# Optimization experiments

Hardware: AMD Instinct MI355X
Metric: run time of the kernel (lower is better)

The kernel has to match this reference:

```python
import jax, jax.numpy as jnp
import numpy as np

B, N, P, E = 64, 512, 256, 4096          # batch, nodes (stations), partition nodes, edges
NUM_NWP, LP, F = 8, 16, 32               # num_nwp, local_points, local_cnn_dims
NT, ED, H, W = 8, 8, 64, 8               # num_temp, edge_feature_dims, decf_mlp_hidden, weight_function_dim
G, RH = 64, 256                          # gnn_dim, readout_hid_dim
H1, Q = 128, 9                           # mlp_hid_dim1, num quantiles


def setup_inputs() -> dict:
    key = jax.random.key(0)
    ks = iter(jax.random.split(key, 40))
    def rn(shape, s=0.05):
        return jax.random.normal(next(ks), shape, dtype=jnp.float32) * s
    # one-hot incidence matrices: each edge has one left (partition) node and one right node
    lidx = jax.random.randint(next(ks), (E,), 0, P)
    ridx = jax.random.randint(next(ks), (E,), 0, N)
    linc = jnp.zeros((P, E), jnp.float32).at[lidx, jnp.arange(E)].set(1.0)
    rinc = jnp.zeros((E, N), jnp.float32).at[jnp.arange(E), ridx].set(1.0)
    inp = {
        "x1": jax.random.normal(next(ks), (B, NUM_NWP * N, LP), dtype=jnp.float32),
        "x2": jax.random.normal(next(ks), (B, NT), dtype=jnp.float32),
        # LocalConv1D grouped conv (torch OIW layout: [Cout, Cin/groups, K])
        "conv_w": rn((F * N, NUM_NWP, LP)), "conv_b": rn((F * N,)),
        # WDSGCN2 edge-weight MLP
        "k1_w": rn((H, ED)), "k1_b": rn((H,)),
        "k2_w": rn((H, NT)),
        "k3_w": rn((H, F)),
        "k4_w": rn((H, F)),
        "k5_w": rn((W, H)), "k5_b": rn((W,)),
        "gc_w": rn((G, F * W)), "gc_b": rn((G,)),
        # readout
        "r0_w": rn((RH, G * P)),
        "r1_w": rn((RH, NT)), "r1_b": rn((RH,)),
        "r2_w": rn((RH, P)),
        "r3_w": rn((P, RH)), "r3_b": rn((P,)),
        # SMlp (forward uses l1 -> ELU -> l3 only)
        "l1_w": rn((H1, NT + G)), "l1_b": rn((H1,)),
        "l3_w": rn((Q, H1)), "l3_b": rn((Q,)),
        # buffers
        "ef": jax.random.normal(next(ks), (E, ED + 1), dtype=jnp.float32),
        "linc": linc,
        "rinc": rinc,
        "cap_feature": jax.random.normal(next(ks), (P,), dtype=jnp.float32),
        "partition_idx": jnp.arange(P, dtype=jnp.int32) * (N // P),
    }
    return inp


def reference(x1, x2, conv_w, conv_b, k1_w, k1_b, k2_w, k3_w, k4_w, k5_w, k5_b,
              gc_w, gc_b, r0_w, r1_w, r1_b, r2_w, r3_w, r3_b,
              l1_w, l1_b, l3_w, l3_b, ef, linc, rinc, cap_feature, partition_idx):
    b = x1.shape[0]
    # --- LocalConv1D: grouped conv1d (valid padding, output length 1) + ReLU ---
    y = jax.lax.conv_general_dilated(x1, conv_w, (1,), 'VALID',
                                     dimension_numbers=('NCH', 'OIH', 'NCH'),
                                     feature_group_count=N)
    x = jax.nn.relu(y + conv_b[None, :, None]).reshape(b, N, F)      # [B,N,F]
    # --- WDSGCN2: per-edge weight kernel ---
    kern = ef[:, :-1] @ k1_w.T + k1_b                                # [E,H]
    kern = kern[None] + (x2 @ k2_w.T)[:, None, :]                    # [B,E,H]
    xp = x[:, partition_idx, :]                                      # [B,P,F]
    kern = kern + jnp.einsum('pe,bpf->bef', linc, xp) @ k3_w.T       # left-node feats
    rx = jnp.einsum('en,bnf->bef', rinc, x)                          # right-node feats [B,E,F]
    kern = kern + rx @ k4_w.T
    kern = jax.nn.relu(jax.nn.leaky_relu(kern, 0.02) @ k5_w.T + k5_b)  # [B,E,W]
    # --- message = kernel (outer) right-node features, aggregated by left incidence ---
    msg = kern[:, :, :, None] * rx[:, :, None, :]                    # [B,E,W,F]
    agg = jnp.einsum('pe,bewf->bpwf', linc, msg).reshape(b, P, W * F)
    yg = jax.nn.relu(agg @ gc_w.T + gc_b)                            # [B,P,G]
    # --- readout attention over partition nodes ---
    h = yg.reshape(b, -1) @ r0_w.T + (x2 @ r1_w.T + r1_b) + cap_feature @ r2_w.T
    wt = jax.nn.relu(jax.nn.leaky_relu(h, 0.01) @ r3_w.T + r3_b)     # [B,P]
    res = jnp.einsum('bp,bpg->bg', wt, yg)                           # [B,G]
    # --- SMlp head ---
    z = jnp.concatenate([res, x2], axis=1)
    z = jax.nn.elu(z @ l1_w.T + l1_b)
    return z @ l3_w.T + l3_b                                         # [B,Q]
```

## Files before the change

kernel.cpp:

```cpp
#include <hip/hip_runtime.h>
#include <math.h>

#define B_ 64
#define N_ 512
#define P_ 256
#define E_ 4096
#define F_ 32
#define H_ 64
#define W_ 8
#define G_ 64
#define RH_ 256

#define X_OFF   0
#define T4_OFF  (X_OFF + N_*B_*F_)
#define T3_OFF  (T4_OFF + N_*B_*H_)
#define KB_OFF  (T3_OFF + P_*B_*H_)
#define KW_OFF  (KB_OFF + E_*H_)
#define YG_OFF  (KW_OFF + E_*B_*W_)
#define HB_OFF  (YG_OFF + B_*P_*G_)
#define RES_OFF (HB_OFF + B_*RH_)
#define INT_OFF (RES_OFF + 4*B_*G_)

__global__ __launch_bounds__(256) void k_decode(const float* __restrict__ linc,
    const float* __restrict__ rinc, int* __restrict__ lidx, int* __restrict__ ridx) {
  int i4 = blockIdx.x * 256 + threadIdx.x;
  const int L4 = (P_ * E_) / 4;
  if (i4 < L4) {
    float4 v = ((const float4*)linc)[i4];
    int i = i4 * 4;
    int p = i >> 12, e = i & 4095;
    if (v.x != 0.0f) lidx[e]     = p;
    if (v.y != 0.0f) lidx[e + 1] = p;
    if (v.z != 0.0f) lidx[e + 2] = p;
    if (v.w != 0.0f) lidx[e + 3] = p;
  } else {
    int j4 = i4 - L4;
    float4 v = ((const float4*)rinc)[j4];
    int j = j4 * 4;
    int e = j >> 9, n = j & 511;
    if (v.x != 0.0f) ridx[e] = n;
    if (v.y != 0.0f) ridx[e] = n + 1;
    if (v.z != 0.0f) ridx[e] = n + 2;
    if (v.w != 0.0f) ridx[e] = n + 3;
  }
}

__global__ __launch_bounds__(1024) void k_lists(const int* __restrict__ lidx,
    int* __restrict__ part_start, int* __restrict__ part_edges) {
  __shared__ int cnt[256];
  __shared__ int buf[256];
  __shared__ int cur[256];
  int t = threadIdx.x;
  if (t < 256) cnt[t] = 0;
  __syncthreads();
  for (int e = t; e < E_; e += 1024) atomicAdd(&cnt[lidx[e]], 1);
  __syncthreads();
  if (t < 256) buf[t] = cnt[t];
  __syncthreads();
  for (int off = 1; off < 256; off <<= 1) {
    int add = 0;
    if (t < 256 && t >= off) add = buf[t - off];
    __syncthreads();
    if (t < 256) buf[t] += add;
    __syncthreads();
  }
  if (t < 256) {
    part_start[t + 1] = buf[t];
    if (t == 0) part_start[0] = 0;
    cur[t] = buf[t] - cnt[t];
  }
  __syncthreads();
  for (int e = t; e < E_; e += 1024) {
    int p = lidx[e];
    int pos = atomicAdd(&cur[p], 1);
    part_edges[pos] = e;
  }
}

__global__ __launch_bounds__(256) void k_conv(const float* __restrict__ x1,
    const float* __restrict__ conv_w, const float* __restrict__ conv_b,
    float* __restrict__ x) {
  __shared__ float wsm[32 * 132];
  __shared__ float xsm[8192];
  int n = blockIdx.x, t = threadIdx.x;
  for (int i = t; i < 1024; i += 256) {
    int f = i >> 5, j = i & 31;
    ((float4*)wsm)[f * 33 + j] = ((const float4*)(conv_w + n * 4096))[i];
  }
  for (int i = t; i < 2048; i += 256) {
    int b = i >> 5, j = i & 31;
    ((float4*)xsm)[i] = ((const float4*)(x1 + b * 65536 + n * 128))[j];
  }
  __syncthreads();
  int f = t & 31, bq = t >> 5;
  float cb = conv_b[n * 32 + f];
  float acc[8];
#pragma unroll
  for (int bi = 0; bi < 8; bi++) acc[bi] = cb;
  const float4* wf4 = (const float4*)wsm + f * 33;
  const float4* xb4 = (const float4*)xsm + bq * 256;
#pragma unroll 4
  for (int k4 = 0; k4 < 32; k4++) {
    float4 wv = wf4[k4];
#pragma unroll
    for (int bi = 0; bi < 8; bi++) {
      float4 xv = xb4[bi * 32 + k4];
      acc[bi] += wv.x * xv.x + wv.y * xv.y + wv.z * xv.z + wv.w * xv.w;
    }
  }
#pragma unroll
  for (int bi = 0; bi < 8; bi++) {
    int b = bq * 8 + bi;
    x[n * 2048 + b * 32 + f] = fmaxf(acc[bi], 0.0f);
  }
}

__global__ __launch_bounds__(256) void k_prep(
    const float* __restrict__ x, const int* __restrict__ pidx,
    const float* __restrict__ k3_w, const float* __restrict__ k4_w,
    const float* __restrict__ x2, const float* __restrict__ k2_w,
    const float* __restrict__ ef, const float* __restrict__ k1_w,
    const float* __restrict__ k1_b,
    const float* __restrict__ r1_w, const float* __restrict__ r1_b,
    const float* __restrict__ r2_w, const float* __restrict__ cap,
    float* __restrict__ t4, float* __restrict__ t3, float* __restrict__ kb,
    float* __restrict__ hbuf) {
  __shared__ float xsh[2048];
  __shared__ float wsh[64 * 36];
  __shared__ float x2s[512];
  __shared__ float k2s[512];
  int blk = blockIdx.x, t = threadIdx.x;
  if (blk < 768) {
    bool isT4 = blk < 512;
    int n = isT4 ? blk : pidx[blk - 512];
    const float* wmat = isT4 ? k4_w : k3_w;
    float* outp = isT4 ? (t4 + blk * 4096) : (t3 + (blk - 512) * 4096);
    for (int i = t; i < 512; i += 256) {
      ((float4*)xsh)[i] = ((const float4*)(x + n * 2048))[i];
      int h = i >> 3, j = i & 7;
      ((float4*)wsh)[h * 9 + j] = ((const float4*)wmat)[i];
    }
    if (isT4) {
      for (int i = t; i < 128; i += 256) {
        ((float4*)x2s)[i] = ((const float4*)x2)[i];
        ((float4*)k2s)[i] = ((const float4*)k2_w)[i];
      }
    }
    __syncthreads();
    int h = t & 63, bq = t >> 6;
    float wreg[32];
#pragma unroll
    for (int j = 0; j < 8; j++) {
      float4 v = ((float4*)wsh)[h * 9 + j];
      wreg[4 * j] = v.x; wreg[4 * j + 1] = v.y; wreg[4 * j + 2] = v.z; wreg[4 * j + 3] = v.w;
    }
    float w2[8];
    if (isT4) {
      float4 u = ((float4*)k2s)[h * 2], v = ((float4*)k2s)[h * 2 + 1];
      w2[0] = u.x; w2[1] = u.y; w2[2] = u.z; w2[3] = u.w;
      w2[4] = v.x; w2[5] = v.y; w2[6] = v.z; w2[7] = v.w;
    }
    for (int bi = 0; bi < 16; bi++) {
      int b = bq * 16 + bi;
      float acc = 0.0f;
#pragma unroll
      for (int j = 0; j < 8; j++) {
        float4 xv = ((float4*)xsh)[b * 8 + j];
        acc += xv.x * wreg[4 * j] + xv.y * wreg[4 * j + 1] +
               xv.z * wreg[4 * j + 2] + xv.w * wreg[4 * j + 3];
      }
      if (isT4) {
        float4 u = ((float4*)x2s)[b * 2], v = ((float4*)x2s)[b * 2 + 1];
        acc += u.x * w2[0] + u.y * w2[1] + u.z * w2[2] + u.w * w2[3] +
               v.x * w2[4] + v.y * w2[5] + v.z * w2[6] + v.w * w2[7];
      }
      outp[b * 64 + h] = acc;
    }
  } else if (blk < 1792) {
    int o = (blk - 768) * 256 + t;
    int e = o >> 6, h = o & 63;
    float acc = k1_b[h];
    const float* er = ef + e * 9;
    const float* kr = k1_w + h * 8;
#pragma unroll
    for (int d = 0; d < 8; d++) acc += er[d] * kr[d];
    kb[o] = acc;
  } else {
    int o = (blk - 1792) * 256 + t;
    int rh = o & 255;
    float acc = r1_b[rh];
    const float* xr = x2 + (o >> 8) * 8;
    const float* rr = r1_w + rh * 8;
#pragma unroll
    for (int d = 0; d < 8; d++) acc += xr[d] * rr[d];
    const float* r2r = r2_w + rh * 256;
    for (int p4 = 0; p4 < 64; p4++) {
      float4 cv = ((const float4*)cap)[p4];
      float4 rv = ((const float4*)r2r)[p4];
      acc += cv.x * rv.x + cv.y * rv.y + cv.z * rv.z + cv.w * rv.w;
    }
    hbuf[o] = acc;
  }
}

__global__ __launch_bounds__(256) void k_eagg(
    const float* __restrict__ x, const float* __restrict__ kb,
    const float* __restrict__ t3, const float* __restrict__ t4,
    const float* __restrict__ k5_w, const float* __restrict__ k5_b,
    const int* __restrict__ ridx, const int* __restrict__ part_start,
    const int* __restrict__ part_edges,
    const float* __restrict__ gc_w, const float* __restrict__ gc_b,
    float* __restrict__ yg) {
  __shared__ float t3s[64 * 68];
  __shared__ float k5t[4 * 520];
  __shared__ unsigned short accS[64 * 256];
  int p = blockIdx.x, t = threadIdx.x;
  for (int i = t; i < 512; i += 256) {
    int h = i >> 3, w = i & 7;
    float v = k5_w[w * 64 + h];
#pragma unroll
    for (int qq = 0; qq < 4; qq++) k5t[qq * 520 + i] = v;
  }
  for (int i4 = t; i4 < 1024; i4 += 256) {
    float4 v = ((const float4*)(t3 + p * 4096))[i4];
    *(float4*)(t3s + (i4 >> 4) * 68 + (i4 & 15) * 4) = v;
  }
  __syncthreads();
  int s = t & 3, b = t >> 2;
  const float* kq = k5t + s * 520 + s * 128;
  float kb5_0 = k5_b[2 * s], kb5_1 = k5_b[2 * s + 1];
  const float4* t3p = (const float4*)(t3s + b * 68 + s * 16);
  float acc[64];
#pragma unroll
  for (int j = 0; j < 64; j++) acc[j] = 0.0f;
  int s0 = part_start[p], s1 = part_start[p + 1];
  int e = 0, r = 0;
  if (s0 < s1) { e = part_edges[s0]; r = ridx[e]; }
  for (int idx = s0; idx < s1; idx++) {
    int e_n = 0, r_n = 0;
    if (idx + 1 < s1) { e_n = part_edges[idx + 1]; r_n = ridx[e_n]; }
    const float4* xp = (const float4*)(x + r * 2048 + b * 32);
    float4 xv0 = xp[0], xv1 = xp[1], xv2 = xp[2], xv3 = xp[3];
    float4 xv4 = xp[4], xv5 = xp[5], xv6 = xp[6], xv7 = xp[7];
    const float4* kb4 = (const float4*)(kb + e * 64 + s * 16);
    const float4* t44 = (const float4*)(t4 + r * 4096 + b * 64 + s * 16);
    float lk[16];
#pragma unroll
    for (int j4 = 0; j4 < 4; j4++) {
      float4 a = kb4[j4], c = t3p[j4], d = t44[j4];
      float v;
      v = a.x + c.x + d.x; lk[j4 * 4 + 0] = v > 0.0f ? v : 0.02f * v;
      v = a.y + c.y + d.y; lk[j4 * 4 + 1] = v > 0.0f ? v : 0.02f * v;
      v = a.z + c.z + d.z; lk[j4 * 4 + 2] = v > 0.0f ? v : 0.02f * v;
      v = a.w + c.w + d.w; lk[j4 * 4 + 3] = v > 0.0f ? v : 0.02f * v;
    }
    float pw[8] = {0, 0, 0, 0, 0, 0, 0, 0};
#pragma unroll
    for (int j = 0; j < 16; j++) {
      float4 u = *(const float4*)(kq + j * 8);
      float4 v = *(const float4*)(kq + j * 8 + 4);
      float l = lk[j];
      pw[0] += l * u.x; pw[1] += l * u.y; pw[2] += l * u.z; pw[3] += l * u.w;
      pw[4] += l * v.x; pw[5] += l * v.y; pw[6] += l * v.z; pw[7] += l * v.w;
    }
#pragma unroll
    for (int w = 0; w < 8; w++) {
      pw[w] += __shfl_xor(pw[w], 1);
      pw[w] += __shfl_xor(pw[w], 2);
    }
    float kv0 = fmaxf(pw[2 * s] + kb5_0, 0.0f);
    float kv1 = fmaxf(pw[2 * s + 1] + kb5_1, 0.0f);
    float xa[32];
    xa[0] = xv0.x; xa[1] = xv0.y; xa[2] = xv0.z; xa[3] = xv0.w;
    xa[4] = xv1.x; xa[5] = xv1.y; xa[6] = xv1.z; xa[7] = xv1.w;
    xa[8] = xv2.x; xa[9] = xv2.y; xa[10] = xv2.z; xa[11] = xv2.w;
    xa[12] = xv3.x; xa[13] = xv3.y; xa[14] = xv3.z; xa[15] = xv3.w;
    xa[16] = xv4.x; xa[17] = xv4.y; xa[18] = xv4.z; xa[19] = xv4.w;
    xa[20] = xv5.x; xa[21] = xv5.y; xa[22] = xv5.z; xa[23] = xv5.w;
    xa[24] = xv6.x; xa[25] = xv6.y; xa[26] = xv6.z; xa[27] = xv6.w;
    xa[28] = xv7.x; xa[29] = xv7.y; xa[30] = xv7.z; xa[31] = xv7.w;
#pragma unroll
    for (int j = 0; j < 32; j++) acc[j] += kv0 * xa[j];
#pragma unroll
    for (int j = 0; j < 32; j++) acc[32 + j] += kv1 * xa[j];
    e = e_n; r = r_n;
  }
#pragma unroll
  for (int o = 0; o < 8; o++) {
    int koct = s * 8 + o;
    int os = koct ^ (b >> 3);
    unsigned int wds[4];
#pragma unroll
    for (int h = 0; h < 4; h++) {
      unsigned int u0 = __float_as_uint(acc[o * 8 + 2 * h]);
      u0 = u0 + 0x7fffu + ((u0 >> 16) & 1u);
      unsigned int u1 = __float_as_uint(acc[o * 8 + 2 * h + 1]);
      u1 = u1 + 0x7fffu + ((u1 >> 16) & 1u);
      wds[h] = (u0 >> 16) | (u1 & 0xffff0000u);
    }
    int4 pk = make_int4((int)wds[0], (int)wds[1], (int)wds[2], (int)wds[3]);
    *(int4*)(accS + b * 256 + os * 8) = pk;
  }
  __syncthreads();
  int lane = t & 63, wv = t >> 6;
  int bg = lane >> 3, gg = lane & 7;
  int g0 = wv * 16 + gg * 2;
  const float* gw0 = gc_w + g0 * 256;
  const float* gw1 = gc_w + (g0 + 1) * 256;
  float ac[8][2];
#pragma unroll
  for (int i = 0; i < 8; i++) { ac[i][0] = 0.0f; ac[i][1] = 0.0f; }
  for (int oct = 0; oct < 32; oct++) {
    int4 a8[8];
#pragma unroll
    for (int i = 0; i < 8; i++) {
      int row = bg * 8 + i;
      int os = oct ^ bg;
      a8[i] = *(const int4*)(accS + row * 256 + os * 8);
    }
    float4 b0a = *(const float4*)(gw0 + oct * 8);
    float4 b0b = *(const float4*)(gw0 + oct * 8 + 4);
    float4 b1a = *(const float4*)(gw1 + oct * 8);
    float4 b1b = *(const float4*)(gw1 + oct * 8 + 4);
    float bv0[8] = {b0a.x, b0a.y, b0a.z, b0a.w, b0b.x, b0b.y, b0b.z, b0b.w};
    float bv1[8] = {b1a.x, b1a.y, b1a.z, b1a.w, b1b.x, b1b.y, b1b.z, b1b.w};
#pragma unroll
    for (int kk = 0; kk < 8; kk++) {
#pragma unroll
      for (int i = 0; i < 8; i++) {
        int w32;
        switch (kk >> 1) {
          case 0: w32 = a8[i].x; break;
          case 1: w32 = a8[i].y; break;
          case 2: w32 = a8[i].z; break;
          default: w32 = a8[i].w; break;
        }
        unsigned int u = (unsigned int)w32;
        unsigned int bits = (kk & 1) ? (u & 0xffff0000u) : (u << 16);
        float av = __uint_as_float(bits);
        ac[i][0] += av * bv0[kk];
        ac[i][1] += av * bv1[kk];
      }
    }
  }
  float gb0 = gc_b[g0], gb1 = gc_b[g0 + 1];
#pragma unroll
  for (int i = 0; i < 8; i++) {
    int bb = bg * 8 + i;
    float* yp = yg + bb * 16384 + p * 64;
    yp[g0]     = fmaxf(ac[i][0] + gb0, 0.0f);
    yp[g0 + 1] = fmaxf(ac[i][1] + gb1, 0.0f);
  }
}

__global__ __launch_bounds__(256) void k_r0(const float* __restrict__ yg,
    const float* __restrict__ r0_w, float* __restrict__ part) {
  __shared__ float ygs[64 * 68];
  __shared__ float wts[64 * 260];
  int kc = blockIdx.x, t = threadIdx.x;
  int k0 = kc * 64;
  {
    int c = t >> 4, rr = t & 15;
    for (int rd = 0; rd < 16; rd++) {
      int rh = rd * 16 + rr;
      float4 v = *(const float4*)(r0_w + rh * 16384 + k0 + c * 4);
      wts[(4 * c + 0) * 260 + rh] = v.x;
      wts[(4 * c + 1) * 260 + rh] = v.y;
      wts[(4 * c + 2) * 260 + rh] = v.z;
      wts[(4 * c + 3) * 260 + rh] = v.w;
    }
  }
  {
    int b = t >> 2, kq = t & 3;
    const float* src = yg + b * 16384 + k0 + kq * 16;
#pragma unroll
    for (int u = 0; u < 4; u++) {
      float4 v = *(const float4*)(src + u * 4);
      int kk = kq * 16 + u * 4;
      ygs[(kk + 0) * 68 + b] = v.x;
      ygs[(kk + 1) * 68 + b] = v.y;
      ygs[(kk + 2) * 68 + b] = v.z;
      ygs[(kk + 3) * 68 + b] = v.w;
    }
  }
  __syncthreads();
  int lane = t & 63, wv = t >> 6;
  int b8 = lane & 7, r8 = lane >> 3;
  const float* yp = ygs + b8 * 8;
  const float* wp = wts + wv * 64 + r8 * 8;
  float acc[8][8];
#pragma unroll
  for (int i = 0; i < 8; i++)
#pragma unroll
    for (int j = 0; j < 8; j++) acc[i][j] = 0.0f;
#pragma unroll 2
  for (int k = 0; k < 64; k++) {
    float4 ya = *(const float4*)(yp + k * 68);
    float4 yb = *(const float4*)(yp + k * 68 + 4);
    float4 wa = *(const float4*)(wp + k * 260);
    float4 wb = *(const float4*)(wp + k * 260 + 4);
    float yv[8] = {ya.x, ya.y, ya.z, ya.w, yb.x, yb.y, yb.z, yb.w};
    float wr[8] = {wa.x, wa.y, wa.z, wa.w, wb.x, wb.y, wb.z, wb.w};
#pragma unroll
    for (int i = 0; i < 8; i++)
#pragma unroll
      for (int j = 0; j < 8; j++) acc[i][j] += yv[i] * wr[j];
  }
  float* pb = part + kc * 16384 + wv * 64 + r8 * 8;
#pragma unroll
  for (int i = 0; i < 8; i++) {
    float4 s0 = make_float4(acc[i][0], acc[i][1], acc[i][2], acc[i][3]);
    float4 s1 = make_float4(acc[i][4], acc[i][5], acc[i][6], acc[i][7]);
    float* pp = pb + (b8 * 8 + i) * 256;
    *(float4*)pp = s0;
    *(float4*)(pp + 4) = s1;
  }
}

__global__ __launch_bounds__(256) void k_r0red(const float* __restrict__ part,
    float* __restrict__ hbuf) {
  int blk = blockIdx.x;
  int oq = blk & 63, kq = blk >> 6;
  int o = oq * 256 + threadIdx.x;
  float s = 0.0f;
  const float* pp = part + kq * 64 * 16384 + o;
#pragma unroll 8
  for (int kc = 0; kc < 64; kc++) s += pp[kc * 16384];
  atomicAdd(&hbuf[o], s);
}

__global__ __launch_bounds__(256) void k_wt_res(const float* __restrict__ hbuf,
    const float* __restrict__ r3_w, const float* __restrict__ r3_b,
    const float* __restrict__ yg, float* __restrict__ res4) {
  __shared__ float hs[256];
  __shared__ float wts[64];
  __shared__ float red[256];
  int blk = blockIdx.x;
  int bb = blk >> 2, pq = blk & 3;
  int t = threadIdx.x;
  float hv = hbuf[bb * 256 + t];
  hs[t] = hv > 0.0f ? hv : 0.01f * hv;
  __syncthreads();
  int pl = t >> 2, c = t & 3;
  int pp = pq * 64 + pl;
  const float4* wrow = (const float4*)(r3_w + pp * 256 + c * 64);
  const float4* h4 = (const float4*)(hs) + c * 16;
  float a = 0.0f;
#pragma unroll
  for (int j = 0; j < 16; j++) {
    float4 w4 = wrow[j], hh = h4[j];
    a += hh.x * w4.x + hh.y * w4.y + hh.z * w4.z + hh.w * w4.w;
  }
  a += __shfl_xor(a, 1);
  a += __shfl_xor(a, 2);
  if (c == 0) wts[pl] = fmaxf(a + r3_b[pp], 0.0f);
  __syncthreads();
  int g = t & 63, ch = t >> 6;
  float r = 0.0f;
  const float* ygp = yg + bb * 16384 + pq * 4096 + g;
#pragma unroll
  for (int pi = 0; pi < 16; pi++) {
    int pl2 = ch * 16 + pi;
    r += wts[pl2] * ygp[pl2 * 64];
  }
  red[t] = r;
  __syncthreads();
  if (t < 64)
    res4[pq * 4096 + bb * 64 + t] = red[t] + red[t + 64] + red[t + 128] + red[t + 192];
}

__global__ __launch_bounds__(128) void k_final(const float* __restrict__ res4,
    const float* __restrict__ x2, const float* __restrict__ l1_w,
    const float* __restrict__ l1_b, const float* __restrict__ l3_w,
    const float* __restrict__ l3_b, float* __restrict__ out) {
  __shared__ float zs[128];
  int bb = blockIdx.x, t = threadIdx.x;
  float acc = l1_b[t];
  const float* wrow = l1_w + t * 72;
  const float* rr = res4 + bb * 64;
#pragma unroll 8
  for (int j = 0; j < 64; j++) {
    float rv = rr[j] + rr[4096 + j] + rr[8192 + j] + rr[12288 + j];
    acc += rv * wrow[j];
  }
  const float* xr = x2 + bb * 8;
#pragma unroll
  for (int j = 0; j < 8; j++) acc += xr[j] * wrow[64 + j];
  zs[t] = acc > 0.0f ? acc : expm1f(acc);
  __syncthreads();
  if (t < 9) {
    float o = l3_b[t];
    const float* w3 = l3_w + t * 128;
    for (int j = 0; j < 128; j++) o += zs[j] * w3[j];
    out[bb * 9 + t] = o;
  }
}

extern "C" void kernel_launch(void* const* d_in, const int* in_sizes, int n_in,
                              void* d_out, int out_size, void* d_ws, size_t ws_size,
                              hipStream_t stream) {
  (void)in_sizes; (void)n_in; (void)out_size; (void)ws_size;
  const float* x1     = (const float*)d_in[0];
  const float* x2     = (const float*)d_in[1];
  const float* conv_w = (const float*)d_in[2];
  const float* conv_b = (const float*)d_in[3];
  const float* k1_w   = (const float*)d_in[4];
  const float* k1_b   = (const float*)d_in[5];
  const float* k2_w   = (const float*)d_in[6];
  const float* k3_w   = (const float*)d_in[7];
  const float* k4_w   = (const float*)d_in[8];
  const float* k5_w   = (const float*)d_in[9];
  const float* k5_b   = (const float*)d_in[10];
  const float* gc_w   = (const float*)d_in[11];
  const float* gc_b   = (const float*)d_in[12];
  const float* r0_w   = (const float*)d_in[13];
  const float* r1_w   = (const float*)d_in[14];
  const float* r1_b   = (const float*)d_in[15];
  const float* r2_w   = (const float*)d_in[16];
  const float* r3_w   = (const float*)d_in[17];
  const float* r3_b   = (const float*)d_in[18];
  const float* l1_w   = (const float*)d_in[19];
  const float* l1_b   = (const float*)d_in[20];
  const float* l3_w   = (const float*)d_in[21];
  const float* l3_b   = (const float*)d_in[22];
  const float* ef     = (const float*)d_in[23];
  const float* linc   = (const float*)d_in[24];
  const float* rinc   = (const float*)d_in[25];
  const float* cap    = (const float*)d_in[26];
  const int*   pidx   = (const int*)d_in[27];
  float* out = (float*)d_out;

  float* ws   = (float*)d_ws;
  float* xbuf = ws + X_OFF;
  float* t4   = ws + T4_OFF;
  float* t3   = ws + T3_OFF;
  float* kb   = ws + KB_OFF;
  float* yg   = ws + YG_OFF;
  float* hbuf = ws + HB_OFF;
  float* res4 = ws + RES_OFF;
  float* part = ws + X_OFF;
  int* ib = (int*)(ws + INT_OFF);
  int* lidx = ib;
  int* ridx = ib + 4096;
  int* part_start = ib + 8192;
  int* part_edges = ib + 8704;

  hipLaunchKernelGGL(k_decode, dim3(3072), dim3(256), 0, stream, linc, rinc, lidx, ridx);
  hipLaunchKernelGGL(k_lists, dim3(1), dim3(1024), 0, stream, lidx, part_start, part_edges);
  hipLaunchKernelGGL(k_conv, dim3(512), dim3(256), 0, stream, x1, conv_w, conv_b, xbuf);
  hipLaunchKernelGGL(k_prep, dim3(1856), dim3(256), 0, stream,
                     xbuf, pidx, k3_w, k4_w, x2, k2_w, ef, k1_w, k1_b,
                     r1_w, r1_b, r2_w, cap, t4, t3, kb, hbuf);
  hipLaunchKernelGGL(k_eagg, dim3(256), dim3(256), 0, stream,
                     xbuf, kb, t3, t4, k5_w, k5_b, ridx, part_start, part_edges,
                     gc_w, gc_b, yg);
  hipLaunchKernelGGL(k_r0, dim3(256), dim3(256), 0, stream, yg, r0_w, part);
  hipLaunchKernelGGL(k_r0red, dim3(256), dim3(256), 0, stream, part, hbuf);
  hipLaunchKernelGGL(k_wt_res, dim3(256), dim3(256), 0, stream, hbuf, r3_w, r3_b, yg, res4);
  hipLaunchKernelGGL(k_final, dim3(64), dim3(128), 0, stream,
                     res4, x2, l1_w, l1_b, l3_w, l3_b, out);
}
```

Baseline: 259.0 us.

## Fuse decode with conv, split edge aggregation across batch, halve r0 split-K chunk

The incidence decode and the local conv now run as one launch, with block ranges choosing the role, which saves a kernel launch. The edge-aggregation kernel is reorganised so each block handles 16 batches of one partition (1024 blocks instead of 256). Each thread owns one hidden-dim quad and reduces the weight-function outputs with a shuffle tree, which cuts registers and raises occupancy. The r0 split-K GEMM uses 32-wide K chunks over 512 blocks, and the partial buffer moves to its own workspace region, so the reduction kernel must now sum twice as many partials.

```diff
diff --git a/kernel.cpp b/kernel.cpp
--- a/kernel.cpp
+++ b/kernel.cpp
@@ -20,28 +20,68 @@
 #define HB_OFF  (YG_OFF + B_*P_*G_)
 #define RES_OFF (HB_OFF + B_*RH_)
 #define INT_OFF (RES_OFF + 4*B_*G_)
-
-__global__ __launch_bounds__(256) void k_decode(const float* __restrict__ linc,
-    const float* __restrict__ rinc, int* __restrict__ lidx, int* __restrict__ ridx) {
-  int i4 = blockIdx.x * 256 + threadIdx.x;
-  const int L4 = (P_ * E_) / 4;
-  if (i4 < L4) {
-    float4 v = ((const float4*)linc)[i4];
-    int i = i4 * 4;
-    int p = i >> 12, e = i & 4095;
-    if (v.x != 0.0f) lidx[e]     = p;
-    if (v.y != 0.0f) lidx[e + 1] = p;
-    if (v.z != 0.0f) lidx[e + 2] = p;
-    if (v.w != 0.0f) lidx[e + 3] = p;
-  } else {
-    int j4 = i4 - L4;
-    float4 v = ((const float4*)rinc)[j4];
-    int j = j4 * 4;
-    int e = j >> 9, n = j & 511;
-    if (v.x != 0.0f) ridx[e] = n;
-    if (v.y != 0.0f) ridx[e] = n + 1;
-    if (v.z != 0.0f) ridx[e] = n + 2;
-    if (v.w != 0.0f) ridx[e] = n + 3;
+#define PART_OFF (INT_OFF + 16384)
+
+__global__ __launch_bounds__(256) void k_dc(const float* __restrict__ linc,
+    const float* __restrict__ rinc, int* __restrict__ lidx, int* __restrict__ ridx,
+    const float* __restrict__ x1, const float* __restrict__ conv_w,
+    const float* __restrict__ conv_b, float* __restrict__ x) {
+  __shared__ float wsm[32 * 132];
+  __shared__ float xsm[8192];
+  int blk = blockIdx.x, t = threadIdx.x;
+  if (blk < 3072) {
+    int i4 = blk * 256 + t;
+    const int L4 = (P_ * E_) / 4;
+    if (i4 < L4) {
+      float4 v = ((const float4*)linc)[i4];
+      int i = i4 * 4;
+      int p = i >> 12, e = i & 4095;
+      if (v.x != 0.0f) lidx[e]     = p;
+      if (v.y != 0.0f) lidx[e + 1] = p;
+      if (v.z != 0.0f) lidx[e + 2] = p;
+      if (v.w != 0.0f) lidx[e + 3] = p;
+    } else {
+      int j4 = i4 - L4;
+      float4 v = ((const float4*)rinc)[j4];
+      int j = j4 * 4;
+      int e = j >> 9, n = j & 511;
+      if (v.x != 0.0f) ridx[e] = n;
+      if (v.y != 0.0f) ridx[e] = n + 1;
+      if (v.z != 0.0f) ridx[e] = n + 2;
+      if (v.w != 0.0f) ridx[e] = n + 3;
+    }
+    return;
+  }
+  int n = blk - 3072;
+  for (int i = t; i < 1024; i += 256) {
+    int f = i >> 5, j = i & 31;
+    ((float4*)wsm)[f * 33 + j] = ((const float4*)(conv_w + n * 4096))[i];
+  }
+  for (int i = t; i < 2048; i += 256) {
+    int b = i >> 5, j = i & 31;
+    ((float4*)xsm)[i] = ((const float4*)(x1 + b * 65536 + n * 128))[j];
+  }
+  __syncthreads();
+  int f = t & 31, bq = t >> 5;
+  float cb = conv_b[n * 32 + f];
+  float acc[8];
+#pragma unroll
+  for (int bi = 0; bi < 8; bi++) acc[bi] = cb;
+  const float4* wf4 = (const float4*)wsm + f * 33;
+  const float4* xb4 = (const float4*)xsm + bq * 256;
+#pragma unroll 4
+  for (int k4 = 0; k4 < 32; k4++) {
+    float4 wv = wf4[k4];
+#pragma unroll
+    for (int bi = 0; bi < 8; bi++) {
+      float4 xv = xb4[bi * 32 + k4];
+      acc[bi] += wv.x * xv.x + wv.y * xv.y + wv.z * xv.z + wv.w * xv.w;
+    }
+  }
+#pragma unroll
+  for (int bi = 0; bi < 8; bi++) {
+    int b = bq * 8 + bi;
+    x[n * 2048 + b * 32 + f] = fmaxf(acc[bi], 0.0f);
   }
 }
 
@@ -74,44 +114,6 @@
     int p = lidx[e];
     int pos = atomicAdd(&cur[p], 1);
     part_edges[pos] = e;
-  }
-}
-
-__global__ __launch_bounds__(256) void k_conv(const float* __restrict__ x1,
-    const float* __restrict__ conv_w, const float* __restrict__ conv_b,
-    float* __restrict__ x) {
-  __shared__ float wsm[32 * 132];
-  __shared__ float xsm[8192];
-  int n = blockIdx.x, t = threadIdx.x;
-  for (int i = t; i < 1024; i += 256) {
-    int f = i >> 5, j = i & 31;
-    ((float4*)wsm)[f * 33 + j] = ((const float4*)(conv_w + n * 4096))[i];
-  }
-  for (int i = t; i < 2048; i += 256) {
-    int b = i >> 5, j = i & 31;
-    ((float4*)xsm)[i] = ((const float4*)(x1 + b * 65536 + n * 128))[j];
-  }
-  __syncthreads();
-  int f = t & 31, bq = t >> 5;
-  float cb = conv_b[n * 32 + f];
-  float acc[8];
-#pragma unroll
-  for (int bi = 0; bi < 8; bi++) acc[bi] = cb;
-  const float4* wf4 = (const float4*)wsm + f * 33;
-  const float4* xb4 = (const float4*)xsm + bq * 256;
-#pragma unroll 4
-  for (int k4 = 0; k4 < 32; k4++) {
-    float4 wv = wf4[k4];
-#pragma unroll
-    for (int bi = 0; bi < 8; bi++) {
-      float4 xv = xb4[bi * 32 + k4];
-      acc[bi] += wv.x * xv.x + wv.y * xv.y + wv.z * xv.z + wv.w * xv.w;
-    }
-  }
-#pragma unroll
-  for (int bi = 0; bi < 8; bi++) {
-    int b = bq * 8 + bi;
-    x[n * 2048 + b * 32 + f] = fmaxf(acc[bi], 0.0f);
   }
 }
 
@@ -211,158 +213,126 @@
     const int* __restrict__ part_edges,
     const float* __restrict__ gc_w, const float* __restrict__ gc_b,
     float* __restrict__ yg) {
-  __shared__ float t3s[64 * 68];
-  __shared__ float k5t[4 * 520];
-  __shared__ unsigned short accS[64 * 256];
-  int p = blockIdx.x, t = threadIdx.x;
-  for (int i = t; i < 512; i += 256) {
-    int h = i >> 3, w = i & 7;
-    float v = k5_w[w * 64 + h];
-#pragma unroll
-    for (int qq = 0; qq < 4; qq++) k5t[qq * 520 + i] = v;
-  }
-  for (int i4 = t; i4 < 1024; i4 += 256) {
-    float4 v = ((const float4*)(t3 + p * 4096))[i4];
-    *(float4*)(t3s + (i4 >> 4) * 68 + (i4 & 15) * 4) = v;
-  }
-  __syncthreads();
-  int s = t & 3, b = t >> 2;
-  const float* kq = k5t + s * 520 + s * 128;
-  float kb5_0 = k5_b[2 * s], kb5_1 = k5_b[2 * s + 1];
-  const float4* t3p = (const float4*)(t3s + b * 68 + s * 16);
-  float acc[64];
-#pragma unroll
-  for (int j = 0; j < 64; j++) acc[j] = 0.0f;
+  __shared__ unsigned short accS[16 * 256];
+  int blk = blockIdx.x, t = threadIdx.x;
+  int p = blk & 255, bsub = blk >> 8;
+  int bl = t >> 4, u = t & 15;
+  int b = bsub * 16 + bl;
+  int w = u & 7, fh = u >> 3;
+  int u0 = u & 1, u1 = (u >> 1) & 1, u2 = (u >> 2) & 1;
+  float4 t3v = *(const float4*)(t3 + p * 4096 + b * 64 + u * 4);
+  float4 k5r[8];
+#pragma unroll
+  for (int ww = 0; ww < 8; ww++) k5r[ww] = *(const float4*)(k5_w + ww * 64 + u * 4);
+  float kb5 = k5_b[w];
+  float acc[16];
+#pragma unroll
+  for (int j = 0; j < 16; j++) acc[j] = 0.0f;
   int s0 = part_start[p], s1 = part_start[p + 1];
   int e = 0, r = 0;
   if (s0 < s1) { e = part_edges[s0]; r = ridx[e]; }
   for (int idx = s0; idx < s1; idx++) {
     int e_n = 0, r_n = 0;
     if (idx + 1 < s1) { e_n = part_edges[idx + 1]; r_n = ridx[e_n]; }
-    const float4* xp = (const float4*)(x + r * 2048 + b * 32);
+    const float4* xp = (const float4*)(x + r * 2048 + b * 32 + fh * 16);
     float4 xv0 = xp[0], xv1 = xp[1], xv2 = xp[2], xv3 = xp[3];
-    float4 xv4 = xp[4], xv5 = xp[5], xv6 = xp[6], xv7 = xp[7];
-    const float4* kb4 = (const float4*)(kb + e * 64 + s * 16);
-    const float4* t44 = (const float4*)(t4 + r * 4096 + b * 64 + s * 16);
-    float lk[16];
-#pragma unroll
-    for (int j4 = 0; j4 < 4; j4++) {
-      float4 a = kb4[j4], c = t3p[j4], d = t44[j4];
-      float v;
-      v = a.x + c.x + d.x; lk[j4 * 4 + 0] = v > 0.0f ? v : 0.02f * v;
-      v = a.y + c.y + d.y; lk[j4 * 4 + 1] = v > 0.0f ? v : 0.02f * v;
-      v = a.z + c.z + d.z; lk[j4 * 4 + 2] = v > 0.0f ? v : 0.02f * v;
-      v = a.w + c.w + d.w; lk[j4 * 4 + 3] = v > 0.0f ? v : 0.02f * v;
-    }
-    float pw[8] = {0, 0, 0, 0, 0, 0, 0, 0};
-#pragma unroll
-    for (int j = 0; j < 16; j++) {
-      float4 u = *(const float4*)(kq + j * 8);
-      float4 v = *(const float4*)(kq + j * 8 + 4);
-      float l = lk[j];
-      pw[0] += l * u.x; pw[1] += l * u.y; pw[2] += l * u.z; pw[3] += l * u.w;
-      pw[4] += l * v.x; pw[5] += l * v.y; pw[6] += l * v.z; pw[7] += l * v.w;
-    }
-#pragma unroll
-    for (int w = 0; w < 8; w++) {
-      pw[w] += __shfl_xor(pw[w], 1);
-      pw[w] += __shfl_xor(pw[w], 2);
-    }
-    float kv0 = fmaxf(pw[2 * s] + kb5_0, 0.0f);
-    float kv1 = fmaxf(pw[2 * s + 1] + kb5_1, 0.0f);
-    float xa[32];
+    float4 kbv = *(const float4*)(kb + e * 64 + u * 4);
+    float4 t4v = *(const float4*)(t4 + r * 4096 + b * 64 + u * 4);
+    float lk[4], v;
+    v = kbv.x + t3v.x + t4v.x; lk[0] = v > 0.0f ? v : 0.02f * v;
+    v = kbv.y + t3v.y + t4v.y; lk[1] = v > 0.0f ? v : 0.02f * v;
+    v = kbv.z + t3v.z + t4v.z; lk[2] = v > 0.0f ? v : 0.02f * v;
+    v = kbv.w + t3v.w + t4v.w; lk[3] = v > 0.0f ? v : 0.02f * v;
+    float pw[8];
+#pragma unroll
+    for (int ww = 0; ww < 8; ww++)
+      pw[ww] = lk[0] * k5r[ww].x + lk[1] * k5r[ww].y +
+               lk[2] * k5r[ww].z + lk[3] * k5r[ww].w;
+    float q[4];
+#pragma unroll
+    for (int i = 0; i < 4; i++)
+      q[i] = pw[2 * i + u0] + __shfl_xor(pw[2 * i + 1 - u0], 1);
+    float rr2[2];
+#pragma unroll
+    for (int j = 0; j < 2; j++)
+      rr2[j] = q[2 * j + u1] + __shfl_xor(q[2 * j + 1 - u1], 2);
+    float sv = rr2[u2] + __shfl_xor(rr2[1 - u2], 4);
+    sv = sv + __shfl_xor(sv, 8);
+    float kv = fmaxf(sv + kb5, 0.0f);
+    float xa[16];
     xa[0] = xv0.x; xa[1] = xv0.y; xa[2] = xv0.z; xa[3] = xv0.w;
     xa[4] = xv1.x; xa[5] = xv1.y; xa[6] = xv1.z; xa[7] = xv1.w;
     xa[8] = xv2.x; xa[9] = xv2.y; xa[10] = xv2.z; xa[11] = xv2.w;
     xa[12] = xv3.x; xa[13] = xv3.y; xa[14] = xv3.z; xa[15] = xv3.w;
-    xa[16] = xv4.x; xa[17] = xv4.y; xa[18] = xv4.z; xa[19] = xv4.w;
-    xa[20] = xv5.x; xa[21] = xv5.y; xa[22] = xv5.z; xa[23] = xv5.w;
-    xa[24] = xv6.x; xa[25] = xv6.y; xa[26] = xv6.z; xa[27] = xv6.w;
-    xa[28] = xv7.x; xa[29] = xv7.y; xa[30] = xv7.z; xa[31] = xv7.w;
-#pragma unroll
-    for (int j = 0; j < 32; j++) acc[j] += kv0 * xa[j];
-#pragma unroll
-    for (int j = 0; j < 32; j++) acc[32 + j] += kv1 * xa[j];
+#pragma unroll
+    for (int j = 0; j < 16; j++) acc[j] += kv * xa[j];
     e = e_n; r = r_n;
   }
-#pragma unroll
-  for (int o = 0; o < 8; o++) {
-    int koct = s * 8 + o;
-    int os = koct ^ (b >> 3);
+  int swz = 4 * (bl & 3);
+  int o0 = w * 4 + fh * 2;
+#pragma unroll
+  for (int half = 0; half < 2; half++) {
     unsigned int wds[4];
 #pragma unroll
-    for (int h = 0; h < 4; h++) {
-      unsigned int u0 = __float_as_uint(acc[o * 8 + 2 * h]);
-      u0 = u0 + 0x7fffu + ((u0 >> 16) & 1u);
-      unsigned int u1 = __float_as_uint(acc[o * 8 + 2 * h + 1]);
-      u1 = u1 + 0x7fffu + ((u1 >> 16) & 1u);
-      wds[h] = (u0 >> 16) | (u1 & 0xffff0000u);
+    for (int h2 = 0; h2 < 4; h2++) {
+      unsigned int a0 = __float_as_uint(acc[half * 8 + 2 * h2]);
+      a0 = a0 + 0x7fffu + ((a0 >> 16) & 1u);
+      unsigned int a1 = __float_as_uint(acc[half * 8 + 2 * h2 + 1]);
+      a1 = a1 + 0x7fffu + ((a1 >> 16) & 1u);
+      wds[h2] = (a0 >> 16) | (a1 & 0xffff0000u);
     }
     int4 pk = make_int4((int)wds[0], (int)wds[1], (int)wds[2], (int)wds[3]);
-    *(int4*)(accS + b * 256 + os * 8) = pk;
+    *(int4*)(accS + bl * 256 + ((o0 + half) ^ swz) * 8) = pk;
   }
   __syncthreads();
   int lane = t & 63, wv = t >> 6;
-  int bg = lane >> 3, gg = lane & 7;
+  int bq = lane >> 3, gg = lane & 7;
   int g0 = wv * 16 + gg * 2;
   const float* gw0 = gc_w + g0 * 256;
-  const float* gw1 = gc_w + (g0 + 1) * 256;
-  float ac[8][2];
-#pragma unroll
-  for (int i = 0; i < 8; i++) { ac[i][0] = 0.0f; ac[i][1] = 0.0f; }
+  const float* gw1 = gw0 + 256;
+  float ac00 = 0.0f, ac01 = 0.0f, ac10 = 0.0f, ac11 = 0.0f;
+  int row0 = bq * 2, row1 = bq * 2 + 1;
+  int sz0 = 4 * (row0 & 3), sz1 = 4 * (row1 & 3);
   for (int oct = 0; oct < 32; oct++) {
-    int4 a8[8];
-#pragma unroll
-    for (int i = 0; i < 8; i++) {
-      int row = bg * 8 + i;
-      int os = oct ^ bg;
-      a8[i] = *(const int4*)(accS + row * 256 + os * 8);
-    }
+    int4 a0 = *(const int4*)(accS + row0 * 256 + (oct ^ sz0) * 8);
+    int4 a1 = *(const int4*)(accS + row1 * 256 + (oct ^ sz1) * 8);
     float4 b0a = *(const float4*)(gw0 + oct * 8);
     float4 b0b = *(const float4*)(gw0 + oct * 8 + 4);
     float4 b1a = *(const float4*)(gw1 + oct * 8);
     float4 b1b = *(const float4*)(gw1 + oct * 8 + 4);
     float bv0[8] = {b0a.x, b0a.y, b0a.z, b0a.w, b0b.x, b0b.y, b0b.z, b0b.w};
     float bv1[8] = {b1a.x, b1a.y, b1a.z, b1a.w, b1b.x, b1b.y, b1b.z, b1b.w};
+    int w32[4] = {a0.x, a0.y, a0.z, a0.w};
+    int w33[4] = {a1.x, a1.y, a1.z, a1.w};
 #pragma unroll
     for (int kk = 0; kk < 8; kk++) {
-#pragma unroll
-      for (int i = 0; i < 8; i++) {
-        int w32;
-        switch (kk >> 1) {
-          case 0: w32 = a8[i].x; break;
-          case 1: w32 = a8[i].y; break;
-          case 2: w32 = a8[i].z; break;
-          default: w32 = a8[i].w; break;
-        }
-        unsigned int u = (unsigned int)w32;
-        unsigned int bits = (kk & 1) ? (u & 0xffff0000u) : (u << 16);
-        float av = __uint_as_float(bits);
-        ac[i][0] += av * bv0[kk];
-        ac[i][1] += av * bv1[kk];
-      }
+      unsigned int uu0 = (unsigned int)w32[kk >> 1];
+      unsigned int uu1 = (unsigned int)w33[kk >> 1];
+      float av0 = __uint_as_float((kk & 1) ? (uu0 & 0xffff0000u) : (uu0 << 16));
+      float av1 = __uint_as_float((kk & 1) ? (uu1 & 0xffff0000u) : (uu1 << 16));
+      ac00 += av0 * bv0[kk]; ac01 += av0 * bv1[kk];
+      ac10 += av1 * bv0[kk]; ac11 += av1 * bv1[kk];
     }
   }
   float gb0 = gc_b[g0], gb1 = gc_b[g0 + 1];
-#pragma unroll
-  for (int i = 0; i < 8; i++) {
-    int bb = bg * 8 + i;
-    float* yp = yg + bb * 16384 + p * 64;
-    yp[g0]     = fmaxf(ac[i][0] + gb0, 0.0f);
-    yp[g0 + 1] = fmaxf(ac[i][1] + gb1, 0.0f);
-  }
+  float* yp0 = yg + (bsub * 16 + row0) * 16384 + p * 64;
+  float* yp1 = yg + (bsub * 16 + row1) * 16384 + p * 64;
+  yp0[g0]     = fmaxf(ac00 + gb0, 0.0f);
+  yp0[g0 + 1] = fmaxf(ac01 + gb1, 0.0f);
+  yp1[g0]     = fmaxf(ac10 + gb0, 0.0f);
+  yp1[g0 + 1] = fmaxf(ac11 + gb1, 0.0f);
 }
 
 __global__ __launch_bounds__(256) void k_r0(const float* __restrict__ yg,
     const float* __restrict__ r0_w, float* __restrict__ part) {
-  __shared__ float ygs[64 * 68];
-  __shared__ float wts[64 * 260];
+  __shared__ float ygs[32 * 69];
+  __shared__ float wts[32 * 260];
   int kc = blockIdx.x, t = threadIdx.x;
-  int k0 = kc * 64;
+  int k0 = kc * 32;
   {
-    int c = t >> 4, rr = t & 15;
-    for (int rd = 0; rd < 16; rd++) {
-      int rh = rd * 16 + rr;
+    int c = t >> 5, rr = t & 31;
+    for (int rd = 0; rd < 8; rd++) {
+      int rh = rd * 32 + rr;
       float4 v = *(const float4*)(r0_w + rh * 16384 + k0 + c * 4);
       wts[(4 * c + 0) * 260 + rh] = v.x;
       wts[(4 * c + 1) * 260 + rh] = v.y;
@@ -372,15 +342,15 @@
   }
   {
     int b = t >> 2, kq = t & 3;
-    const float* src = yg + b * 16384 + k0 + kq * 16;
-#pragma unroll
-    for (int u = 0; u < 4; u++) {
-      float4 v = *(const float4*)(src + u * 4);
-      int kk = kq * 16 + u * 4;
-      ygs[(kk + 0) * 68 + b] = v.x;
-      ygs[(kk + 1) * 68 + b] = v.y;
-      ygs[(kk + 2) * 68 + b] = v.z;
-      ygs[(kk + 3) * 68 + b] = v.w;
+    const float* src = yg + b * 16384 + k0 + kq * 8;
+#pragma unroll
+    for (int uu = 0; uu < 2; uu++) {
+      float4 v = *(const float4*)(src + uu * 4);
+      int kk = kq * 8 + uu * 4;
+      ygs[(kk + 0) * 69 + b] = v.x;
+      ygs[(kk + 1) * 69 + b] = v.y;
+      ygs[(kk + 2) * 69 + b] = v.z;
+      ygs[(kk + 3) * 69 + b] = v.w;
     }
   }
   __syncthreads();
@@ -394,9 +364,9 @@
 #pragma unroll
     for (int j = 0; j < 8; j++) acc[i][j] = 0.0f;
 #pragma unroll 2
-  for (int k = 0; k < 64; k++) {
-    float4 ya = *(const float4*)(yp + k * 68);
-    float4 yb = *(const float4*)(yp + k * 68 + 4);
+  for (int k = 0; k < 32; k++) {
+    float4 ya = *(const float4*)(yp + k * 69);
+    float4 yb = *(const float4*)(yp + k * 69 + 4);
     float4 wa = *(const float4*)(wp + k * 260);
     float4 wb = *(const float4*)(wp + k * 260 + 4);
     float yv[8] = {ya.x, ya.y, ya.z, ya.w, yb.x, yb.y, yb.z, yb.w};
@@ -538,24 +508,24 @@
   float* yg   = ws + YG_OFF;
   float* hbuf = ws + HB_OFF;
   float* res4 = ws + RES_OFF;
-  float* part = ws + X_OFF;
+  float* part = ws + PART_OFF;
   int* ib = (int*)(ws + INT_OFF);
   int* lidx = ib;
   int* ridx = ib + 4096;
   int* part_start = ib + 8192;
   int* part_edges = ib + 8704;
 
-  hipLaunchKernelGGL(k_decode, dim3(3072), dim3(256), 0, stream, linc, rinc, lidx, ridx);
+  hipLaunchKernelGGL(k_dc, dim3(3584), dim3(256), 0, stream,
+                     linc, rinc, lidx, ridx, x1, conv_w, conv_b, xbuf);
   hipLaunchKernelGGL(k_lists, dim3(1), dim3(1024), 0, stream, lidx, part_start, part_edges);
-  hipLaunchKernelGGL(k_conv, dim3(512), dim3(256), 0, stream, x1, conv_w, conv_b, xbuf);
   hipLaunchKernelGGL(k_prep, dim3(1856), dim3(256), 0, stream,
                      xbuf, pidx, k3_w, k4_w, x2, k2_w, ef, k1_w, k1_b,
                      r1_w, r1_b, r2_w, cap, t4, t3, kb, hbuf);
-  hipLaunchKernelGGL(k_eagg, dim3(256), dim3(256), 0, stream,
+  hipLaunchKernelGGL(k_eagg, dim3(1024), dim3(256), 0, stream,
                      xbuf, kb, t3, t4, k5_w, k5_b, ridx, part_start, part_edges,
                      gc_w, gc_b, yg);
-  hipLaunchKernelGGL(k_r0, dim3(256), dim3(256), 0, stream, yg, r0_w, part);
-  hipLaunchKernelGGL(k_r0red, dim3(256), dim3(256), 0, stream, part, hbuf);
+  hipLaunchKernelGGL(k_r0, dim3(512), dim3(256), 0, stream, yg, r0_w, part);
+  hipLaunchKernelGGL(k_r0red, dim3(512), dim3(256), 0, stream, part, hbuf);
   hipLaunchKernelGGL(k_wt_res, dim3(256), dim3(256), 0, stream, hbuf, r3_w, r3_b, yg, res4);
   hipLaunchKernelGGL(k_final, dim3(64), dim3(128), 0, stream,
                      res4, x2, l1_w, l1_b, l3_w, l3_b, out);
```

Result: slower. 294.9 us (+13.9%).
